# Optimization experiments

Hardware: AMD Instinct MI355X
Metric: run time of the kernel (lower is better)

Reference implementation:

```python
import jax, jax.numpy as jnp
import numpy as np

N, IN_DIM, OUT_DIM, HEADS = 50000, 256, 256, 8
C = OUT_DIM // HEADS  # per-head channels = 32
E = 800000
G = 64  # number of graphs in the batch
NEG_SLOPE = 0.2
GN_EPS = 1e-5


def setup_inputs() -> dict:
    key = jax.random.key(0)
    ks = jax.random.split(key, 12)
    x = jax.random.normal(ks[0], (N, IN_DIM), dtype=jnp.float32)
    edge_index = jax.random.randint(ks[1], (2, E), 0, N, dtype=jnp.int64)
    batch = jnp.sort(jax.random.randint(ks[2], (N,), 0, G, dtype=jnp.int64))
    s = 1.0 / np.sqrt(IN_DIM)
    W_l = jax.random.uniform(ks[3], (IN_DIM, HEADS * C), jnp.float32, -s, s)
    b_l = jnp.zeros((HEADS * C,), jnp.float32)
    W_r = jax.random.uniform(ks[4], (IN_DIM, HEADS * C), jnp.float32, -s, s)
    b_r = jnp.zeros((HEADS * C,), jnp.float32)
    att = jax.random.normal(ks[5], (HEADS, C), dtype=jnp.float32) / np.sqrt(C)
    bias = jnp.zeros((HEADS * C,), jnp.float32)
    gn_weight = jnp.ones((OUT_DIM,), jnp.float32)
    gn_bias = jnp.zeros((OUT_DIM,), jnp.float32)
    gn_mean_scale = jnp.ones((OUT_DIM,), jnp.float32)
    return {"x": x, "edge_index": edge_index, "batch": batch,
            "W_l": W_l, "b_l": b_l, "W_r": W_r, "b_r": b_r,
            "att": att, "bias": bias, "gn_weight": gn_weight,
            "gn_bias": gn_bias, "gn_mean_scale": gn_mean_scale}


def _gat_block(x, src, dst, batch, W_l, b_l, W_r, b_r, att, bias,
               gn_weight, gn_bias, gn_mean_scale):
    n = x.shape[0]
    # GATv2Conv (add_self_loops=True, concat=True)
    loops = jnp.arange(n, dtype=src.dtype)
    src = jnp.concatenate([src, loops])
    dst = jnp.concatenate([dst, loops])
    xl = (x @ W_l + b_l).reshape(n, HEADS, C)  # source transform
    xr = (x @ W_r + b_r).reshape(n, HEADS, C)  # target transform
    e = jax.nn.leaky_relu(xl[src] + xr[dst], NEG_SLOPE)  # [E', H, C]
    logits = jnp.einsum('ehc,hc->eh', e, att)            # [E', H]
    # segment softmax over incoming edges of each destination node
    m = jax.ops.segment_max(logits, dst, num_segments=n)
    alpha = jnp.exp(logits - m[dst])
    denom = jax.ops.segment_sum(alpha, dst, num_segments=n)
    alpha = alpha / (denom[dst] + 1e-16)
    msg = xl[src] * alpha[:, :, None]                    # [E', H, C]
    h = jax.ops.segment_sum(msg, dst, num_segments=n).reshape(n, HEADS * C) + bias
    # identity residual (in_dim == out_dim) + ELU
    h = jax.nn.elu(h + x)
    # GraphNorm (post-norm)
    counts = jnp.maximum(jax.ops.segment_sum(jnp.ones((n,), h.dtype), batch,
                                             num_segments=G), 1.0)
    mean = jax.ops.segment_sum(h, batch, num_segments=G) / counts[:, None]
    out0 = h - gn_mean_scale * mean[batch]
    var = jax.ops.segment_sum(out0 * out0, batch, num_segments=G) / counts[:, None]
    return gn_weight * out0 / jnp.sqrt(var[batch] + GN_EPS) + gn_bias


def reference(x, edge_index, batch, W_l, b_l, W_r, b_r, att, bias,
              gn_weight, gn_bias, gn_mean_scale):
    return _gat_block(x, edge_index[0], edge_index[1], batch,
                      W_l, b_l, W_r, b_r, att, bias,
                      gn_weight, gn_bias, gn_mean_scale)
```

## Files before the change

kernel.cpp:

```cpp
#include <hip/hip_runtime.h>
#include <hip/hip_bf16.h>
#include <stdint.h>

#define N_NODES 50000
#define MPAD    50048
#define IN_DIM  256
#define EDGES   800000
#define EPRIME  (EDGES + N_NODES)
#define NGRAPH  64
#define GN_EPS  1e-5f
#define ECPAD   53248
#define MSG_BLOCKS 2048
#define MSG_WAVES  (MSG_BLOCKS * 4)

typedef __attribute__((ext_vector_type(8))) short short8;
typedef __attribute__((ext_vector_type(4))) float floatx4;
typedef __attribute__((ext_vector_type(2))) float float2v;

__device__ __forceinline__ uint32_t pk2bf(float a, float b) {
    union { __hip_bfloat162 h; uint32_t u; } cv;
    cv.h = __float22bfloat162_rn(make_float2(a, b));
    return cv.u;
}

__device__ __forceinline__ unsigned short f2b(float f) {
    uint32_t u = __float_as_uint(f);
    u += 0x7fffu + ((u >> 16) & 1u);
    return (unsigned short)(u >> 16);
}

__device__ __forceinline__ float2v up2(uint32_t u) {
    float2v r;
    r[0] = __uint_as_float(u << 16);
    r[1] = __uint_as_float(u & 0xffff0000u);
    return r;
}

__global__ __launch_bounds__(256) void k_prep_w(const float* __restrict__ Wl,
                                                const float* __restrict__ Wr,
                                                unsigned short* __restrict__ Wt) {
    int idx = blockIdx.x * 256 + threadIdx.x;
    int n = idx >> 8, k = idx & 255;
    float v = (n < 256) ? Wl[k * 256 + n] : Wr[k * 256 + (n - 256)];
    Wt[idx] = f2b(v);
}

__global__ __launch_bounds__(512) void k_gemm(const float* __restrict__ x,
                                              const unsigned short* __restrict__ Wt,
                                              const float* __restrict__ bl,
                                              const float* __restrict__ br,
                                              unsigned short* __restrict__ XL,
                                              unsigned short* __restrict__ XR) {
    __shared__ unsigned short As[64 * 256];
    int rbase = blockIdx.x * 64;
    int tid = threadIdx.x;

#pragma unroll
    for (int it = 0; it < 4; ++it) {
        int c = it * 512 + tid;
        int row = c >> 5, ch = c & 31;
        int gr = rbase + row;
        float4 f0, f1;
        if (gr < N_NODES) {
            const float4* src = (const float4*)(x + (size_t)gr * 256 + ch * 8);
            f0 = src[0]; f1 = src[1];
        } else {
            f0 = make_float4(0.f,0.f,0.f,0.f); f1 = f0;
        }
        uint32_t p0 = pk2bf(f0.x, f0.y), p1 = pk2bf(f0.z, f0.w);
        uint32_t p2 = pk2bf(f1.x, f1.y), p3 = pk2bf(f1.z, f1.w);
        uint4 hv = make_uint4(p0, p1, p2, p3);
        *(uint4*)(As + row * 256 + (ch ^ (row & 7)) * 8) = hv;
    }
    __syncthreads();

    int w = tid >> 6;
    int l = tid & 63;
    int m = l & 15, q = l >> 4;

    floatx4 acc[4][4];
#pragma unroll
    for (int rf = 0; rf < 4; ++rf)
#pragma unroll
        for (int cf = 0; cf < 4; ++cf)
            acc[rf][cf] = (floatx4){0.f, 0.f, 0.f, 0.f};

    const unsigned short* wbase = Wt + (size_t)(w * 64) * 256;

#pragma unroll
    for (int kk = 0; kk < 8; ++kk) {
        short8 a[4];
#pragma unroll
        for (int rf = 0; rf < 4; ++rf) {
            int row = rf * 16 + m;
            int ch = (kk * 4 + q) ^ (row & 7);
            a[rf] = *(const short8*)(As + row * 256 + ch * 8);
        }
#pragma unroll
        for (int cf = 0; cf < 4; ++cf) {
            short8 b = *(const short8*)(wbase + (size_t)(cf * 16 + m) * 256 + kk * 32 + q * 8);
#pragma unroll
            for (int rf = 0; rf < 4; ++rf)
                acc[rf][cf] = __builtin_amdgcn_mfma_f32_16x16x32_bf16(b, a[rf], acc[rf][cf], 0, 0, 0);
        }
    }

    unsigned short* obase = (w < 4) ? XL : XR;
    const float* bptr = (w < 4) ? bl : br;
    int cb = (w & 3) * 64;
#pragma unroll
    for (int cf = 0; cf < 4; ++cf) {
        int chb = cb + cf * 16 + q * 4;
        float4 bv = *(const float4*)(bptr + chb);
#pragma unroll
        for (int rf = 0; rf < 4; ++rf) {
            int node = rbase + rf * 16 + m;
            uint2 o;
            o.x = pk2bf(acc[rf][cf][0] + bv.x, acc[rf][cf][1] + bv.y);
            o.y = pk2bf(acc[rf][cf][2] + bv.z, acc[rf][cf][3] + bv.w);
            *(uint2*)(obase + (size_t)node * 256 + chb) = o;
        }
    }
}

__global__ __launch_bounds__(256) void k_hist(const int* __restrict__ ei,
                                              const int* __restrict__ batch,
                                              int* __restrict__ ecount,
                                              int* __restrict__ ncount,
                                              int* __restrict__ sedge) {
    __shared__ int hist[NGRAPH];
    if (threadIdx.x < NGRAPH) hist[threadIdx.x] = 0;
    __syncthreads();
    int e = blockIdx.x * 256 + threadIdx.x;
    if (e < EPRIME) {
        int d = (e < EDGES) ? ei[EDGES + e] : (e - EDGES);
        atomicAdd(&ecount[d], 1);
    }
    if (e < N_NODES) atomicAdd(&hist[batch[e]], 1);
    if (blockIdx.x == 0 && threadIdx.x < 192) sedge[EPRIME + threadIdx.x] = 0;
    __syncthreads();
    if (threadIdx.x < NGRAPH && hist[threadIdx.x])
        atomicAdd(&ncount[threadIdx.x], hist[threadIdx.x]);
}

__global__ __launch_bounds__(1024) void k_scan_all(const int* __restrict__ ecount,
                                                   int* __restrict__ estart,
                                                   int* __restrict__ ecursor) {
    __shared__ int wsum[16];
    int t = threadIdx.x, w = t >> 6, l = t & 63;
    int carry = 0;
    for (int base = 0; base < ECPAD; base += 4096) {
        int4 v = ((const int4*)(ecount + base))[t];
        int s = v.x + v.y + v.z + v.w;
        int sc = s;
#pragma unroll
        for (int off = 1; off < 64; off <<= 1) {
            int n = __shfl_up(sc, off);
            sc += (l >= off) ? n : 0;
        }
        if (l == 63) wsum[w] = sc;
        __syncthreads();
        int woff = 0, ctot = 0;
#pragma unroll
        for (int i = 0; i < 16; ++i) {
            int wi = wsum[i];
            woff += (i < w) ? wi : 0;
            ctot += wi;
        }
        int e0 = carry + woff + (sc - s);
        int4 o;
        o.x = e0; o.y = e0 + v.x; o.z = o.y + v.y; o.w = o.z + v.z;
        ((int4*)(estart  + base))[t] = o;
        ((int4*)(ecursor + base))[t] = o;
        carry += ctot;
        __syncthreads();
    }
}

__global__ __launch_bounds__(256) void k_scatter(const int* __restrict__ ei,
                                                 int* __restrict__ ecursor,
                                                 int* __restrict__ sedge) {
    int e = blockIdx.x * 256 + threadIdx.x;
    if (e >= EPRIME) return;
    int s, d;
    if (e < EDGES) { s = ei[e]; d = ei[EDGES + e]; }
    else           { s = d = e - EDGES; }
    int pos = atomicAdd(&ecursor[d], 1);
    sedge[pos] = s;
}

__global__ __launch_bounds__(256) void k_msg(const unsigned short* __restrict__ XL,
                                             const unsigned short* __restrict__ XRb,
                                             const float* __restrict__ x,
                                             const float* __restrict__ att,
                                             const float* __restrict__ bias,
                                             const int* __restrict__ sedge,
                                             const int* __restrict__ estart,
                                             const int* __restrict__ ecount,
                                             float* __restrict__ out) {
    int l = threadIdx.x & 63;
    int lofs = l * 8;
    int wid = (int)((blockIdx.x * 256 + threadIdx.x) >> 6);

    float4 bvv  = ((const float4*)bias)[l];
    float4 attv = ((const float4*)att)[l];
    float2v a601 = {0.6f * attv.x, 0.6f * attv.y};
    float2v a623 = {0.6f * attv.z, 0.6f * attv.w};
    float a40 = 0.4f * attv.x, a41 = 0.4f * attv.y;
    float a42 = 0.4f * attv.z, a43 = 0.4f * attv.w;

    for (int d = wid; d < N_NODES; d += MSG_WAVES) {
        float4 xin  = ((const float4*)(x + (size_t)d * 256))[l];
        uint2 xru = ((const uint2*)(XRb + (size_t)d * 256))[l];
        float2v xr01 = up2(xru.x), xr23 = up2(xru.y);

        int s0  = __builtin_amdgcn_readfirstlane(estart[d]);
        int cnt = __builtin_amdgcn_readfirstlane(ecount[d]);

        auto ldrow = [&](int src) -> uint2 {
            size_t off = ((size_t)(uint32_t)__builtin_amdgcn_readfirstlane(src)) << 9;
            return *(const uint2*)((const char*)XL + off + lofs);
        };

        float den0 = 0.f, den1 = 0.f, den2 = 0.f, den3 = 0.f;
        float2v A01 = {0.f,0.f}, A23 = {0.f,0.f};
        float2v B01 = {0.f,0.f}, B23 = {0.f,0.f};
        float2v C01 = {0.f,0.f}, C23 = {0.f,0.f};
        float2v D01 = {0.f,0.f}, D23 = {0.f,0.f};

        auto proc = [&](uint2 U, float& den, float2v& R01, float2v& R23) {
            float2v x01 = up2(U.x), x23 = up2(U.y);
            float2v z01 = x01 + xr01, z23 = x23 + xr23;
            float2v q = z01 * a601 + z23 * a623;
            float t0 = fmaf(fabsf(z01[0]), a40, q[0]);
            float t1 = fmaf(fabsf(z01[1]), a41, q[1]);
            t0 = fmaf(fabsf(z23[0]), a42, t0);
            t1 = fmaf(fabsf(z23[1]), a43, t1);
            float pp = t0 + t1;
            int pi = __float_as_int(pp);
            pp += __int_as_float(__builtin_amdgcn_update_dpp(0, pi, 0xB1, 0xF, 0xF, true));
            pi = __float_as_int(pp);
            pp += __int_as_float(__builtin_amdgcn_update_dpp(0, pi, 0x4E, 0xF, 0xF, true));
            pi = __float_as_int(pp);
            pp += __int_as_float(__builtin_amdgcn_update_dpp(0, pi, 0x141, 0xF, 0xF, true));
            float al = __expf(fminf(pp, 80.f));
            den += al;
            float2v al2 = {al, al};
            R01 += al2 * x01;
            R23 += al2 * x23;
        };

        uint2 P0 = ldrow(sedge[s0]);
        uint2 P1 = ldrow(sedge[s0 + 1]);
        uint2 P2 = ldrow(sedge[s0 + 2]);
        uint2 P3 = ldrow(sedge[s0 + 3]);

        int nq = cnt >> 2;
        for (int qq = 0; qq < nq; ++qq) {
            uint2 Q0 = P0, Q1 = P1, Q2 = P2, Q3 = P3;
            int nb = s0 + (qq + 1) * 4;
            P0 = ldrow(sedge[nb]);
            P1 = ldrow(sedge[nb + 1]);
            P2 = ldrow(sedge[nb + 2]);
            P3 = ldrow(sedge[nb + 3]);
            proc(Q0, den0, A01, A23);
            proc(Q1, den1, B01, B23);
            proc(Q2, den2, C01, C23);
            proc(Q3, den3, D01, D23);
        }
        int rem = cnt & 3;
        if (rem > 0) proc(P0, den0, A01, A23);
        if (rem > 1) proc(P1, den1, B01, B23);
        if (rem > 2) proc(P2, den2, C01, C23);

        float inv = 1.f / ((den0 + den1) + (den2 + den3) + 1e-16f);
        A01 = (A01 + B01) + (C01 + D01);
        A23 = (A23 + B23) + (C23 + D23);

        float h0 = A01[0] * inv + bvv.x + xin.x; h0 = (h0 > 0.f) ? h0 : (__expf(h0) - 1.f);
        float h1 = A01[1] * inv + bvv.y + xin.y; h1 = (h1 > 0.f) ? h1 : (__expf(h1) - 1.f);
        float h2 = A23[0] * inv + bvv.z + xin.z; h2 = (h2 > 0.f) ? h2 : (__expf(h2) - 1.f);
        float h3 = A23[1] * inv + bvv.w + xin.w; h3 = (h3 > 0.f) ? h3 : (__expf(h3) - 1.f);
        ((float4*)(out + (size_t)d * 256))[l] = make_float4(h0, h1, h2, h3);
    }
}

#define GN_ROWS 64
__global__ __launch_bounds__(256) void k_gn_sum(const float* __restrict__ h,
                                                const int* __restrict__ batch,
                                                float* __restrict__ gsum,
                                                float* __restrict__ gsq) {
    __shared__ int bsh[GN_ROWS];
    int r0 = blockIdx.x * GN_ROWS;
    if (threadIdx.x < GN_ROWS) {
        int i = r0 + threadIdx.x;
        bsh[threadIdx.x] = (i < N_NODES) ? batch[i] : -1;
    }
    __syncthreads();
    int c = threadIdx.x;
    float s1 = 0.f, s2 = 0.f;
    int g = bsh[0];
    for (int j = 0; j < GN_ROWS; j += 4) {
        int i = r0 + j;
        if (i >= N_NODES) break;
        bool full = (i + 3 < N_NODES);
        if (full && bsh[j] == g && bsh[j + 3] == g) {
            const float* hp = h + (size_t)i * 256 + c;
            float v0 = hp[0], v1 = hp[256], v2 = hp[512], v3 = hp[768];
            s1 += (v0 + v1) + (v2 + v3);
            s2 += (v0 * v0 + v1 * v1) + (v2 * v2 + v3 * v3);
        } else {
            for (int jj = j; jj < j + 4; ++jj) {
                int ii = r0 + jj;
                if (ii >= N_NODES) break;
                int bg = bsh[jj];
                if (bg != g) {
                    atomicAdd(&gsum[g * 256 + c], s1);
                    atomicAdd(&gsq[g * 256 + c], s2);
                    s1 = 0.f; s2 = 0.f; g = bg;
                }
                float v = h[(size_t)ii * 256 + c];
                s1 += v; s2 += v * v;
            }
        }
    }
    atomicAdd(&gsum[g * 256 + c], s1);
    atomicAdd(&gsq[g * 256 + c], s2);
}

__global__ __launch_bounds__(256) void k_final(float* __restrict__ out,
                                               const int* __restrict__ batch,
                                               const float* __restrict__ gsum,
                                               const float* __restrict__ gsq,
                                               const int* __restrict__ ncount,
                                               const float* __restrict__ gnw,
                                               const float* __restrict__ gnb,
                                               const float* __restrict__ gms) {
    int idx = blockIdx.x * 256 + threadIdx.x;
    int i = idx >> 6, l = idx & 63;
    if (i >= N_NODES) return;
    int g = batch[i];
    float inv = 1.f / fmaxf((float)ncount[g], 1.f);
    float4 hv = ((const float4*)(out + (size_t)i * 256))[l];
    float4 ms = ((const float4*)(gsum + g * 256))[l];
    float4 qs = ((const float4*)(gsq  + g * 256))[l];
    float4 wv = ((const float4*)gnw)[l];
    float4 bv = ((const float4*)gnb)[l];
    float4 sv = ((const float4*)gms)[l];
    float4 o;
    {
        float m = ms.x * inv, q = qs.x * inv;
        o.x = wv.x * (hv.x - sv.x * m) * rsqrtf(q - m * m * sv.x * (2.f - sv.x) + GN_EPS) + bv.x;
    }
    {
        float m = ms.y * inv, q = qs.y * inv;
        o.y = wv.y * (hv.y - sv.y * m) * rsqrtf(q - m * m * sv.y * (2.f - sv.y) + GN_EPS) + bv.y;
    }
    {
        float m = ms.z * inv, q = qs.z * inv;
        o.z = wv.z * (hv.z - sv.z * m) * rsqrtf(q - m * m * sv.z * (2.f - sv.z) + GN_EPS) + bv.z;
    }
    {
        float m = ms.w * inv, q = qs.w * inv;
        o.w = wv.w * (hv.w - sv.w * m) * rsqrtf(q - m * m * sv.w * (2.f - sv.w) + GN_EPS) + bv.w;
    }
    ((float4*)(out + (size_t)i * 256))[l] = o;
}

extern "C" void kernel_launch(void* const* d_in, const int* in_sizes, int n_in,
                              void* d_out, int out_size, void* d_ws, size_t ws_size,
                              hipStream_t stream) {
    const float* x    = (const float*)d_in[0];
    const int*   ei   = (const int*)d_in[1];
    const int*   batch= (const int*)d_in[2];
    const float* Wl   = (const float*)d_in[3];
    const float* bl   = (const float*)d_in[4];
    const float* Wr   = (const float*)d_in[5];
    const float* br   = (const float*)d_in[6];
    const float* att  = (const float*)d_in[7];
    const float* bias = (const float*)d_in[8];
    const float* gnw  = (const float*)d_in[9];
    const float* gnb  = (const float*)d_in[10];
    const float* gms  = (const float*)d_in[11];
    float* out = (float*)d_out;

    char* p = (char*)d_ws;
    auto alloc = [&](size_t bytes) -> char* {
        char* r = p;
        p += (bytes + 255) & ~(size_t)255;
        return r;
    };
    unsigned short* Wt  = (unsigned short*)alloc((size_t)512 * 256 * 2);
    unsigned short* XL  = (unsigned short*)alloc((size_t)MPAD * 256 * 2);
    unsigned short* XRb = (unsigned short*)alloc((size_t)MPAD * 256 * 2);
    int* estart         = (int*)alloc((size_t)ECPAD * 4);
    int* ecursor        = (int*)alloc((size_t)ECPAD * 4);
    int* sedge          = (int*)alloc((size_t)(EPRIME + 192) * 4);
    int* ecount         = (int*)alloc((size_t)ECPAD * 4);
    int* ncount         = (int*)alloc((size_t)NGRAPH * 4);
    float* gsum         = (float*)alloc((size_t)2 * NGRAPH * 256 * 4);
    float* gsq          = gsum + NGRAPH * 256;
    size_t zbytes = (size_t)((char*)(gsum + 2 * NGRAPH * 256) - (char*)ecount);
    hipMemsetAsync(ecount, 0, zbytes, stream);

    k_prep_w<<<512, 256, 0, stream>>>(Wl, Wr, Wt);
    k_gemm<<<MPAD / 64, 512, 0, stream>>>(x, Wt, bl, br, XL, XRb);

    k_hist<<<(EPRIME + 255) / 256, 256, 0, stream>>>(ei, batch, ecount, ncount, sedge);
    k_scan_all<<<1, 1024, 0, stream>>>(ecount, estart, ecursor);
    k_scatter<<<(EPRIME + 255) / 256, 256, 0, stream>>>(ei, ecursor, sedge);

    k_msg<<<MSG_BLOCKS, 256, 0, stream>>>(XL, XRb, x, att, bias,
                                          sedge, estart, ecount, out);

    k_gn_sum<<<(N_NODES + GN_ROWS - 1) / GN_ROWS, 256, 0, stream>>>(out, batch, gsum, gsq);
    k_final<<<N_NODES * 64 / 256, 256, 0, stream>>>(out, batch, gsum, gsq,
                                                    ncount, gnw, gnb, gms);
}
```

Before: 369.4 us.

## Fuse weight prep with histogram, deepen message prefetch, vectorize GraphNorm reductions

Merges the weight transpose/bf16 conversion and the edge/graph histogram into one launch, removing a kernel boundary. The message kernel switches from a grid-stride loop to one wave per node and prefetches eight neighbor rows instead of four to hide more gather latency. The GraphNorm sum kernel now uses float4 loads with a shared-memory reduction across waves, which cuts atomic traffic in blocks that hold a single graph. The final normalize kernel becomes a grid-stride loop over 2048 blocks, and each of these parts adds register pressure or changes occupancy.

```diff
diff --git a/kernel.cpp b/kernel.cpp
--- a/kernel.cpp
+++ b/kernel.cpp
@@ -10,8 +10,8 @@
 #define NGRAPH  64
 #define GN_EPS  1e-5f
 #define ECPAD   53248
-#define MSG_BLOCKS 2048
-#define MSG_WAVES  (MSG_BLOCKS * 4)
+#define HIST_BLOCKS 3321
+#define PREP_BLOCKS 512
 
 typedef __attribute__((ext_vector_type(8))) short short8;
 typedef __attribute__((ext_vector_type(4))) float floatx4;
@@ -36,13 +36,34 @@
     return r;
 }
 
-__global__ __launch_bounds__(256) void k_prep_w(const float* __restrict__ Wl,
-                                                const float* __restrict__ Wr,
-                                                unsigned short* __restrict__ Wt) {
-    int idx = blockIdx.x * 256 + threadIdx.x;
-    int n = idx >> 8, k = idx & 255;
-    float v = (n < 256) ? Wl[k * 256 + n] : Wr[k * 256 + (n - 256)];
-    Wt[idx] = f2b(v);
+__global__ __launch_bounds__(256) void k_pre(const float* __restrict__ Wl,
+                                             const float* __restrict__ Wr,
+                                             unsigned short* __restrict__ Wt,
+                                             const int* __restrict__ ei,
+                                             const int* __restrict__ batch,
+                                             int* __restrict__ ecount,
+                                             int* __restrict__ ncount,
+                                             int* __restrict__ sedge) {
+    if (blockIdx.x < PREP_BLOCKS) {
+        int idx = blockIdx.x * 256 + threadIdx.x;
+        int n = idx >> 8, k = idx & 255;
+        float v = (n < 256) ? Wl[k * 256 + n] : Wr[k * 256 + (n - 256)];
+        Wt[idx] = f2b(v);
+        return;
+    }
+    __shared__ int hist[NGRAPH];
+    if (threadIdx.x < NGRAPH) hist[threadIdx.x] = 0;
+    __syncthreads();
+    int e = (blockIdx.x - PREP_BLOCKS) * 256 + threadIdx.x;
+    if (e < EPRIME) {
+        int d = (e < EDGES) ? ei[EDGES + e] : (e - EDGES);
+        atomicAdd(&ecount[d], 1);
+    }
+    if (e < N_NODES) atomicAdd(&hist[batch[e]], 1);
+    if (blockIdx.x == PREP_BLOCKS && threadIdx.x < 192) sedge[EPRIME + threadIdx.x] = 0;
+    __syncthreads();
+    if (threadIdx.x < NGRAPH && hist[threadIdx.x])
+        atomicAdd(&ncount[threadIdx.x], hist[threadIdx.x]);
 }
 
 __global__ __launch_bounds__(512) void k_gemm(const float* __restrict__ x,
@@ -123,26 +144,6 @@
     }
 }
 
-__global__ __launch_bounds__(256) void k_hist(const int* __restrict__ ei,
-                                              const int* __restrict__ batch,
-                                              int* __restrict__ ecount,
-                                              int* __restrict__ ncount,
-                                              int* __restrict__ sedge) {
-    __shared__ int hist[NGRAPH];
-    if (threadIdx.x < NGRAPH) hist[threadIdx.x] = 0;
-    __syncthreads();
-    int e = blockIdx.x * 256 + threadIdx.x;
-    if (e < EPRIME) {
-        int d = (e < EDGES) ? ei[EDGES + e] : (e - EDGES);
-        atomicAdd(&ecount[d], 1);
-    }
-    if (e < N_NODES) atomicAdd(&hist[batch[e]], 1);
-    if (blockIdx.x == 0 && threadIdx.x < 192) sedge[EPRIME + threadIdx.x] = 0;
-    __syncthreads();
-    if (threadIdx.x < NGRAPH && hist[threadIdx.x])
-        atomicAdd(&ncount[threadIdx.x], hist[threadIdx.x]);
-}
-
 __global__ __launch_bounds__(1024) void k_scan_all(const int* __restrict__ ecount,
                                                    int* __restrict__ estart,
                                                    int* __restrict__ ecursor) {
@@ -198,10 +199,11 @@
                                              const int* __restrict__ estart,
                                              const int* __restrict__ ecount,
                                              float* __restrict__ out) {
+    int d = (int)((blockIdx.x * 256 + threadIdx.x) >> 6);
     int l = threadIdx.x & 63;
     int lofs = l * 8;
-    int wid = (int)((blockIdx.x * 256 + threadIdx.x) >> 6);
-
+
+    float4 xin  = ((const float4*)(x + (size_t)d * 256))[l];
     float4 bvv  = ((const float4*)bias)[l];
     float4 attv = ((const float4*)att)[l];
     float2v a601 = {0.6f * attv.x, 0.6f * attv.y};
@@ -209,80 +211,94 @@
     float a40 = 0.4f * attv.x, a41 = 0.4f * attv.y;
     float a42 = 0.4f * attv.z, a43 = 0.4f * attv.w;
 
-    for (int d = wid; d < N_NODES; d += MSG_WAVES) {
-        float4 xin  = ((const float4*)(x + (size_t)d * 256))[l];
-        uint2 xru = ((const uint2*)(XRb + (size_t)d * 256))[l];
-        float2v xr01 = up2(xru.x), xr23 = up2(xru.y);
-
-        int s0  = __builtin_amdgcn_readfirstlane(estart[d]);
-        int cnt = __builtin_amdgcn_readfirstlane(ecount[d]);
-
-        auto ldrow = [&](int src) -> uint2 {
-            size_t off = ((size_t)(uint32_t)__builtin_amdgcn_readfirstlane(src)) << 9;
-            return *(const uint2*)((const char*)XL + off + lofs);
-        };
-
-        float den0 = 0.f, den1 = 0.f, den2 = 0.f, den3 = 0.f;
-        float2v A01 = {0.f,0.f}, A23 = {0.f,0.f};
-        float2v B01 = {0.f,0.f}, B23 = {0.f,0.f};
-        float2v C01 = {0.f,0.f}, C23 = {0.f,0.f};
-        float2v D01 = {0.f,0.f}, D23 = {0.f,0.f};
-
-        auto proc = [&](uint2 U, float& den, float2v& R01, float2v& R23) {
-            float2v x01 = up2(U.x), x23 = up2(U.y);
-            float2v z01 = x01 + xr01, z23 = x23 + xr23;
-            float2v q = z01 * a601 + z23 * a623;
-            float t0 = fmaf(fabsf(z01[0]), a40, q[0]);
-            float t1 = fmaf(fabsf(z01[1]), a41, q[1]);
-            t0 = fmaf(fabsf(z23[0]), a42, t0);
-            t1 = fmaf(fabsf(z23[1]), a43, t1);
-            float pp = t0 + t1;
-            int pi = __float_as_int(pp);
-            pp += __int_as_float(__builtin_amdgcn_update_dpp(0, pi, 0xB1, 0xF, 0xF, true));
-            pi = __float_as_int(pp);
-            pp += __int_as_float(__builtin_amdgcn_update_dpp(0, pi, 0x4E, 0xF, 0xF, true));
-            pi = __float_as_int(pp);
-            pp += __int_as_float(__builtin_amdgcn_update_dpp(0, pi, 0x141, 0xF, 0xF, true));
-            float al = __expf(fminf(pp, 80.f));
-            den += al;
-            float2v al2 = {al, al};
-            R01 += al2 * x01;
-            R23 += al2 * x23;
-        };
-
-        uint2 P0 = ldrow(sedge[s0]);
-        uint2 P1 = ldrow(sedge[s0 + 1]);
-        uint2 P2 = ldrow(sedge[s0 + 2]);
-        uint2 P3 = ldrow(sedge[s0 + 3]);
-
-        int nq = cnt >> 2;
-        for (int qq = 0; qq < nq; ++qq) {
-            uint2 Q0 = P0, Q1 = P1, Q2 = P2, Q3 = P3;
-            int nb = s0 + (qq + 1) * 4;
-            P0 = ldrow(sedge[nb]);
-            P1 = ldrow(sedge[nb + 1]);
-            P2 = ldrow(sedge[nb + 2]);
-            P3 = ldrow(sedge[nb + 3]);
-            proc(Q0, den0, A01, A23);
-            proc(Q1, den1, B01, B23);
-            proc(Q2, den2, C01, C23);
-            proc(Q3, den3, D01, D23);
-        }
-        int rem = cnt & 3;
-        if (rem > 0) proc(P0, den0, A01, A23);
-        if (rem > 1) proc(P1, den1, B01, B23);
-        if (rem > 2) proc(P2, den2, C01, C23);
-
-        float inv = 1.f / ((den0 + den1) + (den2 + den3) + 1e-16f);
-        A01 = (A01 + B01) + (C01 + D01);
-        A23 = (A23 + B23) + (C23 + D23);
-
-        float h0 = A01[0] * inv + bvv.x + xin.x; h0 = (h0 > 0.f) ? h0 : (__expf(h0) - 1.f);
-        float h1 = A01[1] * inv + bvv.y + xin.y; h1 = (h1 > 0.f) ? h1 : (__expf(h1) - 1.f);
-        float h2 = A23[0] * inv + bvv.z + xin.z; h2 = (h2 > 0.f) ? h2 : (__expf(h2) - 1.f);
-        float h3 = A23[1] * inv + bvv.w + xin.w; h3 = (h3 > 0.f) ? h3 : (__expf(h3) - 1.f);
-        ((float4*)(out + (size_t)d * 256))[l] = make_float4(h0, h1, h2, h3);
-    }
+    uint2 xru = ((const uint2*)(XRb + (size_t)d * 256))[l];
+    float2v xr01 = up2(xru.x), xr23 = up2(xru.y);
+
+    int s0  = __builtin_amdgcn_readfirstlane(estart[d]);
+    int cnt = __builtin_amdgcn_readfirstlane(ecount[d]);
+
+    auto ldrow = [&](int src) -> uint2 {
+        size_t off = ((size_t)(uint32_t)__builtin_amdgcn_readfirstlane(src)) << 9;
+        return *(const uint2*)((const char*)XL + off + lofs);
+    };
+
+    float den0 = 0.f, den1 = 0.f, den2 = 0.f, den3 = 0.f;
+    float2v A01 = {0.f,0.f}, A23 = {0.f,0.f};
+    float2v B01 = {0.f,0.f}, B23 = {0.f,0.f};
+    float2v C01 = {0.f,0.f}, C23 = {0.f,0.f};
+    float2v D01 = {0.f,0.f}, D23 = {0.f,0.f};
+
+    auto proc = [&](uint2 U, float& den, float2v& R01, float2v& R23) {
+        float2v x01 = up2(U.x), x23 = up2(U.y);
+        float2v z01 = x01 + xr01, z23 = x23 + xr23;
+        float2v q = z01 * a601 + z23 * a623;
+        float t0 = fmaf(fabsf(z01[0]), a40, q[0]);
+        float t1 = fmaf(fabsf(z01[1]), a41, q[1]);
+        t0 = fmaf(fabsf(z23[0]), a42, t0);
+        t1 = fmaf(fabsf(z23[1]), a43, t1);
+        float pp = t0 + t1;
+        int pi = __float_as_int(pp);
+        pp += __int_as_float(__builtin_amdgcn_update_dpp(0, pi, 0xB1, 0xF, 0xF, true));
+        pi = __float_as_int(pp);
+        pp += __int_as_float(__builtin_amdgcn_update_dpp(0, pi, 0x4E, 0xF, 0xF, true));
+        pi = __float_as_int(pp);
+        pp += __int_as_float(__builtin_amdgcn_update_dpp(0, pi, 0x141, 0xF, 0xF, true));
+        float al = __expf(fminf(pp, 80.f));
+        den += al;
+        float2v al2 = {al, al};
+        R01 += al2 * x01;
+        R23 += al2 * x23;
+    };
+
+    uint2 P0 = ldrow(sedge[s0]);
+    uint2 P1 = ldrow(sedge[s0 + 1]);
+    uint2 P2 = ldrow(sedge[s0 + 2]);
+    uint2 P3 = ldrow(sedge[s0 + 3]);
+    uint2 P4 = ldrow(sedge[s0 + 4]);
+    uint2 P5 = ldrow(sedge[s0 + 5]);
+    uint2 P6 = ldrow(sedge[s0 + 6]);
+    uint2 P7 = ldrow(sedge[s0 + 7]);
+
+    int nq = cnt >> 3;
+    for (int qq = 0; qq < nq; ++qq) {
+        uint2 Q0 = P0, Q1 = P1, Q2 = P2, Q3 = P3;
+        uint2 Q4 = P4, Q5 = P5, Q6 = P6, Q7 = P7;
+        int nb = s0 + (qq + 1) * 8;
+        P0 = ldrow(sedge[nb]);
+        P1 = ldrow(sedge[nb + 1]);
+        P2 = ldrow(sedge[nb + 2]);
+        P3 = ldrow(sedge[nb + 3]);
+        P4 = ldrow(sedge[nb + 4]);
+        P5 = ldrow(sedge[nb + 5]);
+        P6 = ldrow(sedge[nb + 6]);
+        P7 = ldrow(sedge[nb + 7]);
+        proc(Q0, den0, A01, A23);
+        proc(Q1, den1, B01, B23);
+        proc(Q2, den2, C01, C23);
+        proc(Q3, den3, D01, D23);
+        proc(Q4, den0, A01, A23);
+        proc(Q5, den1, B01, B23);
+        proc(Q6, den2, C01, C23);
+        proc(Q7, den3, D01, D23);
+    }
+    int rem = cnt & 7;
+    if (rem > 0) proc(P0, den0, A01, A23);
+    if (rem > 1) proc(P1, den1, B01, B23);
+    if (rem > 2) proc(P2, den2, C01, C23);
+    if (rem > 3) proc(P3, den3, D01, D23);
+    if (rem > 4) proc(P4, den0, A01, A23);
+    if (rem > 5) proc(P5, den1, B01, B23);
+    if (rem > 6) proc(P6, den2, C01, C23);
+
+    float inv = 1.f / ((den0 + den1) + (den2 + den3) + 1e-16f);
+    A01 = (A01 + B01) + (C01 + D01);
+    A23 = (A23 + B23) + (C23 + D23);
+
+    float h0 = A01[0] * inv + bvv.x + xin.x; h0 = (h0 > 0.f) ? h0 : (__expf(h0) - 1.f);
+    float h1 = A01[1] * inv + bvv.y + xin.y; h1 = (h1 > 0.f) ? h1 : (__expf(h1) - 1.f);
+    float h2 = A23[0] * inv + bvv.z + xin.z; h2 = (h2 > 0.f) ? h2 : (__expf(h2) - 1.f);
+    float h3 = A23[1] * inv + bvv.w + xin.w; h3 = (h3 > 0.f) ? h3 : (__expf(h3) - 1.f);
+    ((float4*)(out + (size_t)d * 256))[l] = make_float4(h0, h1, h2, h3);
 }
 
 #define GN_ROWS 64
@@ -291,43 +307,87 @@
                                                 float* __restrict__ gsum,
                                                 float* __restrict__ gsq) {
     __shared__ int bsh[GN_ROWS];
+    __shared__ float4 redS[4][64];
+    __shared__ float4 redQ[4][64];
     int r0 = blockIdx.x * GN_ROWS;
-    if (threadIdx.x < GN_ROWS) {
-        int i = r0 + threadIdx.x;
-        bsh[threadIdx.x] = (i < N_NODES) ? batch[i] : -1;
+    int t = threadIdx.x;
+    if (t < GN_ROWS) {
+        int i = r0 + t;
+        bsh[t] = (i < N_NODES) ? batch[i] : -2;
     }
     __syncthreads();
-    int c = threadIdx.x;
-    float s1 = 0.f, s2 = 0.f;
-    int g = bsh[0];
-    for (int j = 0; j < GN_ROWS; j += 4) {
-        int i = r0 + j;
-        if (i >= N_NODES) break;
-        bool full = (i + 3 < N_NODES);
-        if (full && bsh[j] == g && bsh[j + 3] == g) {
-            const float* hp = h + (size_t)i * 256 + c;
-            float v0 = hp[0], v1 = hp[256], v2 = hp[512], v3 = hp[768];
-            s1 += (v0 + v1) + (v2 + v3);
-            s2 += (v0 * v0 + v1 * v1) + (v2 * v2 + v3 * v3);
-        } else {
-            for (int jj = j; jj < j + 4; ++jj) {
-                int ii = r0 + jj;
-                if (ii >= N_NODES) break;
-                int bg = bsh[jj];
-                if (bg != g) {
-                    atomicAdd(&gsum[g * 256 + c], s1);
-                    atomicAdd(&gsq[g * 256 + c], s2);
-                    s1 = 0.f; s2 = 0.f; g = bg;
-                }
-                float v = h[(size_t)ii * 256 + c];
-                s1 += v; s2 += v * v;
-            }
-        }
-    }
-    atomicAdd(&gsum[g * 256 + c], s1);
-    atomicAdd(&gsq[g * 256 + c], s2);
-}
-
+    int l = t & 63, w = t >> 6;
+    bool uni = (r0 + GN_ROWS <= N_NODES) && (bsh[0] == bsh[GN_ROWS - 1]);
+
+    if (uni) {
+        const float* hp = h + (size_t)(r0 + w) * 256 + l * 4;
+        float4 s1 = make_float4(0.f, 0.f, 0.f, 0.f);
+        float4 s2 = make_float4(0.f, 0.f, 0.f, 0.f);
+#pragma unroll
+        for (int k = 0; k < 16; ++k) {
+            float4 v = *(const float4*)(hp + (size_t)k * 1024);
+            s1.x += v.x; s1.y += v.y; s1.z += v.z; s1.w += v.w;
+            s2.x = fmaf(v.x, v.x, s2.x);
+            s2.y = fmaf(v.y, v.y, s2.y);
+            s2.z = fmaf(v.z, v.z, s2.z);
+            s2.w = fmaf(v.w, v.w, s2.w);
+        }
+        redS[w][l] = s1; redQ[w][l] = s2;
+        __syncthreads();
+        if (w == 0) {
+            float4 b1 = redS[1][l], c1 = redS[2][l], d1 = redS[3][l];
+            float4 b2 = redQ[1][l], c2 = redQ[2][l], d2 = redQ[3][l];
+            s1.x += b1.x + c1.x + d1.x; s1.y += b1.y + c1.y + d1.y;
+            s1.z += b1.z + c1.z + d1.z; s1.w += b1.w + c1.w + d1.w;
+            s2.x += b2.x + c2.x + d2.x; s2.y += b2.y + c2.y + d2.y;
+            s2.z += b2.z + c2.z + d2.z; s2.w += b2.w + c2.w + d2.w;
+            int g = bsh[0];
+            float* gp = gsum + g * 256 + l * 4;
+            atomicAdd(gp + 0, s1.x); atomicAdd(gp + 1, s1.y);
+            atomicAdd(gp + 2, s1.z); atomicAdd(gp + 3, s1.w);
+            float* gq = gsq + g * 256 + l * 4;
+            atomicAdd(gq + 0, s2.x); atomicAdd(gq + 1, s2.y);
+            atomicAdd(gq + 2, s2.z); atomicAdd(gq + 3, s2.w);
+        }
+        return;
+    }
+
+    float4 s1 = make_float4(0.f, 0.f, 0.f, 0.f);
+    float4 s2 = make_float4(0.f, 0.f, 0.f, 0.f);
+    int g = (r0 + w < N_NODES) ? bsh[w] : -1;
+    for (int j = w; j < GN_ROWS; j += 4) {
+        int ii = r0 + j;
+        if (ii >= N_NODES) break;
+        int bg = bsh[j];
+        if (bg != g) {
+            float* gp = gsum + g * 256 + l * 4;
+            atomicAdd(gp + 0, s1.x); atomicAdd(gp + 1, s1.y);
+            atomicAdd(gp + 2, s1.z); atomicAdd(gp + 3, s1.w);
+            float* gq = gsq + g * 256 + l * 4;
+            atomicAdd(gq + 0, s2.x); atomicAdd(gq + 1, s2.y);
+            atomicAdd(gq + 2, s2.z); atomicAdd(gq + 3, s2.w);
+            s1 = make_float4(0.f, 0.f, 0.f, 0.f);
+            s2 = make_float4(0.f, 0.f, 0.f, 0.f);
+            g = bg;
+        }
+        float4 v = *(const float4*)(h + (size_t)ii * 256 + l * 4);
+        s1.x += v.x; s1.y += v.y; s1.z += v.z; s1.w += v.w;
+        s2.x = fmaf(v.x, v.x, s2.x);
+        s2.y = fmaf(v.y, v.y, s2.y);
+        s2.z = fmaf(v.z, v.z, s2.z);
+        s2.w = fmaf(v.w, v.w, s2.w);
+    }
+    if (g >= 0) {
+        float* gp = gsum + g * 256 + l * 4;
+        atomicAdd(gp + 0, s1.x); atomicAdd(gp + 1, s1.y);
+        atomicAdd(gp + 2, s1.z); atomicAdd(gp + 3, s1.w);
+        float* gq = gsq + g * 256 + l * 4;
+        atomicAdd(gq + 0, s2.x); atomicAdd(gq + 1, s2.y);
+        atomicAdd(gq + 2, s2.z); atomicAdd(gq + 3, s2.w);
+    }
+}
+
+#define FIN_BLOCKS 2048
 __global__ __launch_bounds__(256) void k_final(float* __restrict__ out,
                                                const int* __restrict__ batch,
                                                const float* __restrict__ gsum,
@@ -336,35 +396,35 @@
                                                const float* __restrict__ gnw,
                                                const float* __restrict__ gnb,
                                                const float* __restrict__ gms) {
-    int idx = blockIdx.x * 256 + threadIdx.x;
-    int i = idx >> 6, l = idx & 63;
-    if (i >= N_NODES) return;
-    int g = batch[i];
-    float inv = 1.f / fmaxf((float)ncount[g], 1.f);
-    float4 hv = ((const float4*)(out + (size_t)i * 256))[l];
-    float4 ms = ((const float4*)(gsum + g * 256))[l];
-    float4 qs = ((const float4*)(gsq  + g * 256))[l];
+    int l = threadIdx.x & 63, wr = threadIdx.x >> 6;
     float4 wv = ((const float4*)gnw)[l];
     float4 bv = ((const float4*)gnb)[l];
     float4 sv = ((const float4*)gms)[l];
-    float4 o;
-    {
-        float m = ms.x * inv, q = qs.x * inv;
-        o.x = wv.x * (hv.x - sv.x * m) * rsqrtf(q - m * m * sv.x * (2.f - sv.x) + GN_EPS) + bv.x;
-    }
-    {
-        float m = ms.y * inv, q = qs.y * inv;
-        o.y = wv.y * (hv.y - sv.y * m) * rsqrtf(q - m * m * sv.y * (2.f - sv.y) + GN_EPS) + bv.y;
-    }
-    {
-        float m = ms.z * inv, q = qs.z * inv;
-        o.z = wv.z * (hv.z - sv.z * m) * rsqrtf(q - m * m * sv.z * (2.f - sv.z) + GN_EPS) + bv.z;
-    }
-    {
-        float m = ms.w * inv, q = qs.w * inv;
-        o.w = wv.w * (hv.w - sv.w * m) * rsqrtf(q - m * m * sv.w * (2.f - sv.w) + GN_EPS) + bv.w;
-    }
-    ((float4*)(out + (size_t)i * 256))[l] = o;
+    for (int i = blockIdx.x * 4 + wr; i < N_NODES; i += FIN_BLOCKS * 4) {
+        int g = batch[i];
+        float inv = 1.f / fmaxf((float)ncount[g], 1.f);
+        float4 hv = ((const float4*)(out + (size_t)i * 256))[l];
+        float4 ms = ((const float4*)(gsum + g * 256))[l];
+        float4 qs = ((const float4*)(gsq  + g * 256))[l];
+        float4 o;
+        {
+            float m = ms.x * inv, q = qs.x * inv;
+            o.x = wv.x * (hv.x - sv.x * m) * rsqrtf(q - m * m * sv.x * (2.f - sv.x) + GN_EPS) + bv.x;
+        }
+        {
+            float m = ms.y * inv, q = qs.y * inv;
+            o.y = wv.y * (hv.y - sv.y * m) * rsqrtf(q - m * m * sv.y * (2.f - sv.y) + GN_EPS) + bv.y;
+        }
+        {
+            float m = ms.z * inv, q = qs.z * inv;
+            o.z = wv.z * (hv.z - sv.z * m) * rsqrtf(q - m * m * sv.z * (2.f - sv.z) + GN_EPS) + bv.z;
+        }
+        {
+            float m = ms.w * inv, q = qs.w * inv;
+            o.w = wv.w * (hv.w - sv.w * m) * rsqrtf(q - m * m * sv.w * (2.f - sv.w) + GN_EPS) + bv.w;
+        }
+        ((float4*)(out + (size_t)i * 256))[l] = o;
+    }
 }
 
 extern "C" void kernel_launch(void* const* d_in, const int* in_sizes, int n_in,
@@ -403,17 +463,17 @@
     size_t zbytes = (size_t)((char*)(gsum + 2 * NGRAPH * 256) - (char*)ecount);
     hipMemsetAsync(ecount, 0, zbytes, stream);
 
-    k_prep_w<<<512, 256, 0, stream>>>(Wl, Wr, Wt);
+    k_pre<<<PREP_BLOCKS + HIST_BLOCKS, 256, 0, stream>>>(Wl, Wr, Wt, ei, batch,
+                                                         ecount, ncount, sedge);
     k_gemm<<<MPAD / 64, 512, 0, stream>>>(x, Wt, bl, br, XL, XRb);
 
-    k_hist<<<(EPRIME + 255) / 256, 256, 0, stream>>>(ei, batch, ecount, ncount, sedge);
     k_scan_all<<<1, 1024, 0, stream>>>(ecount, estart, ecursor);
-    k_scatter<<<(EPRIME + 255) / 256, 256, 0, stream>>>(ei, ecursor, sedge);
-
-    k_msg<<<MSG_BLOCKS, 256, 0, stream>>>(XL, XRb, x, att, bias,
-                                          sedge, estart, ecount, out);
+    k_scatter<<<HIST_BLOCKS, 256, 0, stream>>>(ei, ecursor, sedge);
+
+    k_msg<<<N_NODES / 4, 256, 0, stream>>>(XL, XRb, x, att, bias,
+                                           sedge, estart, ecount, out);
 
     k_gn_sum<<<(N_NODES + GN_ROWS - 1) / GN_ROWS, 256, 0, stream>>>(out, batch, gsum, gsq);
-    k_final<<<N_NODES * 64 / 256, 256, 0, stream>>>(out, batch, gsum, gsq,
-                                                    ncount, gnw, gnb, gms);
-}
+    k_final<<<FIN_BLOCKS, 256, 0, stream>>>(out, batch, gsum, gsq,
+                                            ncount, gnw, gnb, gms);
+}
```

After: 378.5 us. 1.02x slower.
